# Performance work log

Measured on AMD Instinct MI355X. Metric: run time of the kernel, lower is better.

## Reference

```python
import jax, jax.numpy as jnp
import numpy as np

N, F_IN = 4096, 128
UNITS0, HEADS0 = 16, 4   # hidden GraphAttention layer
UNITS1, HEADS1 = 1, 1    # final layer (sigmoid, mean over last axis)


def _glorot(key, shape):
    fan_in, fan_out = shape[0], shape[1]
    std = (2.0 / (fan_in + fan_out)) ** 0.5
    return std * jax.random.normal(key, shape, dtype=jnp.float32)


def setup_inputs() -> dict:
    key = jax.random.key(0)
    ks = jax.random.split(key, 8)
    x = jax.random.normal(ks[0], (N, F_IN), dtype=jnp.float32)
    adj = (jax.random.uniform(ks[1], (N, N)) < 0.01).astype(jnp.float32)
    return {
        "x": x,
        "adj": adj,
        "w0": _glorot(ks[2], (F_IN, UNITS0)),
        "aw1_0": _glorot(ks[3], (UNITS0, HEADS0)),
        "aw2_0": _glorot(ks[4], (UNITS0, HEADS0)),
        "w1": _glorot(ks[5], (UNITS0 * HEADS0, UNITS1)),
        "aw1_1": _glorot(ks[6], (UNITS1, HEADS1)),
        "aw2_1": _glorot(ks[7], (UNITS1, HEADS1)),
    }


def _gat_layer(x, adj, w, aw1, aw2, activation, final_layer):
    h = x @ w                                   # [N, units]
    a1 = h @ aw1                                # [N, H]
    a2 = h @ aw2                                # [N, H]
    # relu(a1_i + a2_j) broadcast -> [N, N, H]
    coeffs = jax.nn.relu(a1[:, None, :] + a2[None, :, :])
    # elementwise adjacency mask then softmax over neighbor axis (axis=1),
    # matching tf.nn.softmax(adj * coeffs[:,:,i], axis=1)
    attn = jax.nn.softmax(adj[:, :, None] * coeffs, axis=1)   # [N, N, H]
    # per-head aggregation then concat heads: [N, H*units]
    out = jnp.einsum('ijh,jd->ihd', attn, h).reshape(h.shape[0], -1)
    if final_layer:
        out = out.mean(axis=-1)                 # [N]
    return activation(out)


def reference(x, adj, w0, aw1_0, aw2_0, w1, aw1_1, aw2_1):
    h = _gat_layer(x, adj, w0, aw1_0, aw2_0, jax.nn.relu, False)   # [N, 64]
    out = _gat_layer(h, adj, w1, aw1_1, aw2_1, jax.nn.sigmoid, True)  # [N]
    return out
```

## Files before the change

### kernel.cpp

```cpp
#include <hip/hip_runtime.h>
#include <hip/hip_bf16.h>

#define N 4096
#define FIN 128
#define U0 16
#define H0 4
#define MAXD 128
#define NGEMM (N / 16)

__global__ void k1_fused(const float* __restrict__ adj, const float* __restrict__ x,
                         const float* __restrict__ w0, const float* __restrict__ aw1,
                         const float* __restrict__ aw2,
                         int* __restrict__ deg, int* __restrict__ cols,
                         float* __restrict__ h0, float* __restrict__ a1,
                         float* __restrict__ a2, float* __restrict__ partS0) {
    const int t = threadIdx.x;
    if (blockIdx.x < NGEMM) {
        const int bid = blockIdx.x;
        __shared__ float xs[16][FIN + 1];
        __shared__ float ws[FIN][U0];
        __shared__ float hs[16][U0 + 1];
        const int r0 = bid * 16;

        for (int k = t; k < FIN * U0; k += 256) ws[k / U0][k % U0] = w0[k];
        for (int k = t; k < 16 * FIN; k += 256)
            xs[k / FIN][k % FIN] = x[(size_t)(r0 + k / FIN) * FIN + (k % FIN)];
        __syncthreads();

        const int r = t / U0, u = t % U0;
        float acc = 0.f;
        #pragma unroll 8
        for (int k = 0; k < FIN; ++k) acc += xs[r][k] * ws[k][u];
        hs[r][u] = acc;
        h0[(size_t)(r0 + r) * U0 + u] = acc;
        __syncthreads();

        if (t < 16 * H0) {
            const int rr = t / H0, hh = t % H0;
            float s1 = 0.f, s2 = 0.f;
            #pragma unroll
            for (int u2 = 0; u2 < U0; ++u2) {
                float hv = hs[rr][u2];
                s1 += hv * aw1[u2 * H0 + hh];
                s2 += hv * aw2[u2 * H0 + hh];
            }
            a1[(r0 + rr) * H0 + hh] = s1;
            a2[(r0 + rr) * H0 + hh] = s2;
        } else if (t >= 128 && t < 144) {
            const int d = t - 128;
            float s = 0.f;
            #pragma unroll
            for (int rr = 0; rr < 16; ++rr) s += hs[rr][d];
            partS0[bid * 16 + d] = s;
        }
    } else {
        const int row = blockIdx.x - NGEMM;
        const int lane = t & 63, wid = t >> 6;
        const float4* __restrict__ arow =
            reinterpret_cast<const float4*>(adj + (size_t)row * N);

        __shared__ int cls[MAXD];
        __shared__ int wsum[4];
        __shared__ int dgs;

        float4 v[4];
        int c = 0;
        #pragma unroll
        for (int p = 0; p < 4; ++p) {
            v[p] = arow[t + 256 * p];
            c += (v[p].x != 0.f) + (v[p].y != 0.f) + (v[p].z != 0.f) + (v[p].w != 0.f);
        }

        int sc = c;
        #pragma unroll
        for (int s = 1; s < 64; s <<= 1) {
            int u = __shfl_up(sc, s);
            if (lane >= s) sc += u;
        }
        if (lane == 63) wsum[wid] = sc;
        __syncthreads();
        int base = 0;
        #pragma unroll
        for (int w2 = 0; w2 < 4; ++w2)
            if (w2 < wid) base += wsum[w2];
        const int off = base + sc - c;
        if (t == 255) {
            const int dgv = min(base + sc, MAXD);
            dgs = dgv;
            deg[row] = dgv;
        }

        int w = off;
        #pragma unroll
        for (int p = 0; p < 4; ++p) {
            const int j0 = (t + 256 * p) * 4;
            if (v[p].x != 0.f && w < MAXD) cls[w++] = j0;
            if (v[p].y != 0.f && w < MAXD) cls[w++] = j0 + 1;
            if (v[p].z != 0.f && w < MAXD) cls[w++] = j0 + 2;
            if (v[p].w != 0.f && w < MAXD) cls[w++] = j0 + 3;
        }
        __syncthreads();
        if (t < dgs) cols[(size_t)row * MAXD + t] = cls[t];
    }
}

__global__ void attn0(const float* __restrict__ h0, const float* __restrict__ a1,
                      const float* __restrict__ a2, const float* __restrict__ partS0,
                      const int* __restrict__ deg, const int* __restrict__ cols,
                      const float* __restrict__ w1, float* __restrict__ hp) {
    const int i = blockIdx.x;
    const int t = threadIdx.x;
    __shared__ int cls[MAXD];
    __shared__ float red[16][17];
    __shared__ float s0s[16];
    __shared__ float ln[4][64];
    __shared__ float ld[4][64];

    const int dg = deg[i];
    if (t < MAXD) cls[t] = (t < dg) ? cols[(size_t)i * MAXD + t] : 0;

    {
        const int d = t & 15, ch = t >> 4;
        float s = 0.f;
        #pragma unroll
        for (int k = ch; k < 256; k += 16) s += partS0[k * 16 + d];
        red[ch][d] = s;
    }
    __syncthreads();
    if (t < 16) {
        float s2 = 0.f;
        #pragma unroll
        for (int k = 0; k < 16; ++k) s2 += red[k][t];
        s0s[t] = s2;
    }
    __syncthreads();

    const int wid = t >> 6, lane = t & 63;
    const int hh = lane >> 4, d = lane & 15;
    const float a1v = a1[i * H0 + hh];

    float accn = 0.f, accd = 0.f;
    for (int c = 0; ; ++c) {
        const int kb = wid + 16 * c;
        if (kb >= dg) break;
        int ja[4];
        float ms[4];
        #pragma unroll
        for (int q = 0; q < 4; ++q) {
            const int k = kb + 4 * q;
            ja[q] = cls[k < MAXD ? k : 0];
            ms[q] = (k < dg) ? 1.f : 0.f;
        }
        float a2v[4], h0v[4];
        #pragma unroll
        for (int q = 0; q < 4; ++q) {
            a2v[q] = a2[ja[q] * H0 + hh];
            h0v[q] = h0[(size_t)ja[q] * U0 + d];
        }
        #pragma unroll
        for (int q = 0; q < 4; ++q) {
            float cc = a1v + a2v[q];
            cc = cc > 0.f ? cc : 0.f;
            const float e = (__expf(cc) - 1.f) * ms[q];
            accn = fmaf(e, h0v[q], accn);
            accd += e;
        }
    }
    ln[wid][lane] = accn;
    ld[wid][lane] = accd;
    __syncthreads();

    if (t < 64) {
        const float an = ln[0][t] + ln[1][t] + ln[2][t] + ln[3][t];
        const float ad = ld[0][t] + ld[1][t] + ld[2][t] + ld[3][t];
        float o = (an + s0s[t & 15]) / (ad + (float)N);
        o = o > 0.f ? o : 0.f;

        float pv = o * w1[t];
        #pragma unroll
        for (int off = 32; off; off >>= 1) pv += __shfl_down(pv, off);
        if (t == 0) hp[i] = pv;
    }
}

__global__ void attn1(const float* __restrict__ hp,
                      const float* __restrict__ aw11, const float* __restrict__ aw21,
                      const int* __restrict__ deg, const int* __restrict__ cols,
                      float* __restrict__ out) {
    __shared__ float hps[N];
    __shared__ int cls[4][MAXD];
    __shared__ float s1red[4];
    const int t = threadIdx.x;
    const int w = t >> 6, lane = t & 63;
    const int i0 = blockIdx.x * 4;

    float s = 0.f;
    const float4* __restrict__ hp4 = reinterpret_cast<const float4*>(hp);
    #pragma unroll
    for (int k = t; k < N / 4; k += 256) {
        float4 v = hp4[k];
        reinterpret_cast<float4*>(hps)[k] = v;
        s += v.x + v.y + v.z + v.w;
    }
    for (int k = t; k < 4 * MAXD; k += 256)
        cls[k >> 7][k & 127] = cols[(size_t)(i0 + (k >> 7)) * MAXD + (k & 127)];

    #pragma unroll
    for (int o = 32; o; o >>= 1) s += __shfl_down(s, o);
    if (lane == 0) s1red[w] = s;
    __syncthreads();
    const float S1 = s1red[0] + s1red[1] + s1red[2] + s1red[3];

    const int i = i0 + w;
    const float w1v = aw11[0], w2v = aw21[0];
    const float a1v = hps[i] * w1v;
    const int dg = deg[i];

    float accn = 0.f, accd = 0.f;
    for (int k = lane; k < dg; k += 64) {
        const int j = cls[w][k];
        const float hj = hps[j];
        float cc = a1v + hj * w2v;
        cc = cc > 0.f ? cc : 0.f;
        const float e = __expf(cc) - 1.f;
        accn = fmaf(e, hj, accn);
        accd += e;
    }
    #pragma unroll
    for (int o = 32; o; o >>= 1) {
        accn += __shfl_down(accn, o);
        accd += __shfl_down(accd, o);
    }
    if (lane == 0) {
        const float v = (accn + S1) / (accd + (float)N);
        out[i] = 1.f / (1.f + __expf(-v));
    }
}

extern "C" void kernel_launch(void* const* d_in, const int* in_sizes, int n_in,
                              void* d_out, int out_size, void* d_ws, size_t ws_size,
                              hipStream_t stream) {
    const float* x    = (const float*)d_in[0];
    const float* adj  = (const float*)d_in[1];
    const float* w0   = (const float*)d_in[2];
    const float* aw10 = (const float*)d_in[3];
    const float* aw20 = (const float*)d_in[4];
    const float* w1   = (const float*)d_in[5];
    const float* aw11 = (const float*)d_in[6];
    const float* aw21 = (const float*)d_in[7];
    float* out = (float*)d_out;

    char* p = (char*)d_ws;
    auto alloc = [&](size_t bytes) {
        char* r = p;
        p += (bytes + 255) & ~(size_t)255;
        return r;
    };
    float* partS0 = (float*)alloc(NGEMM * 16 * 4);
    float* h0     = (float*)alloc((size_t)N * U0 * 4);
    float* a1     = (float*)alloc((size_t)N * H0 * 4);
    float* a2     = (float*)alloc((size_t)N * H0 * 4);
    float* hp     = (float*)alloc((size_t)N * 4);
    int*   deg    = (int*)alloc((size_t)N * 4);
    int*   cols   = (int*)alloc((size_t)N * MAXD * 4);

    k1_fused<<<N + NGEMM, 256, 0, stream>>>(adj, x, w0, aw10, aw20,
                                            deg, cols, h0, a1, a2, partS0);
    attn0<<<N, 256, 0, stream>>>(h0, a1, a2, partS0, deg, cols, w1, hp);
    attn1<<<N / 4, 256, 0, stream>>>(hp, aw11, aw21, deg, cols, out);
}
```

Measured before the change: 37.93 us.

## Interleave h0 and a2 into one strided buffer and process two adjacency rows per block

Stores h0 and a2 together in a 32-float-stride feature buffer, so each neighbor gather in attn0 reads one contiguous row instead of two separate arrays. The CSR-building part of k1_fused now handles two adjacency rows per block with 8 float4 loads in flight per thread, halving the block count and raising memory-level parallelism. This costs more registers per thread, an extra barrier, and a larger feature buffer with padding.

After: 38.77 us. 1.02x slower.

```diff
diff --git a/kernel.cpp b/kernel.cpp
--- a/kernel.cpp
+++ b/kernel.cpp
@@ -7,13 +7,15 @@
 #define H0 4
 #define MAXD 128
 #define NGEMM (N / 16)
+#define NCSR (N / 2)
+#define FSTRIDE 32
 
 __global__ void k1_fused(const float* __restrict__ adj, const float* __restrict__ x,
                          const float* __restrict__ w0, const float* __restrict__ aw1,
                          const float* __restrict__ aw2,
                          int* __restrict__ deg, int* __restrict__ cols,
-                         float* __restrict__ h0, float* __restrict__ a1,
-                         float* __restrict__ a2, float* __restrict__ partS0) {
+                         float* __restrict__ F, float* __restrict__ a1,
+                         float* __restrict__ partS0) {
     const int t = threadIdx.x;
     if (blockIdx.x < NGEMM) {
         const int bid = blockIdx.x;
@@ -32,7 +34,7 @@
         #pragma unroll 8
         for (int k = 0; k < FIN; ++k) acc += xs[r][k] * ws[k][u];
         hs[r][u] = acc;
-        h0[(size_t)(r0 + r) * U0 + u] = acc;
+        F[(size_t)(r0 + r) * FSTRIDE + u] = acc;
         __syncthreads();
 
         if (t < 16 * H0) {
@@ -45,7 +47,7 @@
                 s2 += hv * aw2[u2 * H0 + hh];
             }
             a1[(r0 + rr) * H0 + hh] = s1;
-            a2[(r0 + rr) * H0 + hh] = s2;
+            F[(size_t)(r0 + rr) * FSTRIDE + 16 + hh] = s2;
         } else if (t >= 128 && t < 144) {
             const int d = t - 128;
             float s = 0.f;
@@ -54,58 +56,73 @@
             partS0[bid * 16 + d] = s;
         }
     } else {
-        const int row = blockIdx.x - NGEMM;
+        const int rb = (blockIdx.x - NGEMM) * 2;
         const int lane = t & 63, wid = t >> 6;
-        const float4* __restrict__ arow =
-            reinterpret_cast<const float4*>(adj + (size_t)row * N);
-
-        __shared__ int cls[MAXD];
+
+        __shared__ int cls[2][MAXD];
         __shared__ int wsum[4];
-        __shared__ int dgs;
-
-        float4 v[4];
-        int c = 0;
-        #pragma unroll
-        for (int p = 0; p < 4; ++p) {
-            v[p] = arow[t + 256 * p];
-            c += (v[p].x != 0.f) + (v[p].y != 0.f) + (v[p].z != 0.f) + (v[p].w != 0.f);
-        }
-
-        int sc = c;
-        #pragma unroll
-        for (int s = 1; s < 64; s <<= 1) {
-            int u = __shfl_up(sc, s);
-            if (lane >= s) sc += u;
-        }
-        if (lane == 63) wsum[wid] = sc;
+        __shared__ int dgs[2];
+
+        const float4* __restrict__ ar0 =
+            reinterpret_cast<const float4*>(adj + (size_t)rb * N);
+        const float4* __restrict__ ar1 =
+            reinterpret_cast<const float4*>(adj + (size_t)(rb + 1) * N);
+        float4 v0[4], v1[4];
+        #pragma unroll
+        for (int p = 0; p < 4; ++p) v0[p] = ar0[t + 256 * p];
+        #pragma unroll
+        for (int p = 0; p < 4; ++p) v1[p] = ar1[t + 256 * p];
+
+        #pragma unroll
+        for (int rr = 0; rr < 2; ++rr) {
+            const float4* v = rr ? v1 : v0;
+            int c = 0;
+            #pragma unroll
+            for (int p = 0; p < 4; ++p)
+                c += (v[p].x != 0.f) + (v[p].y != 0.f) + (v[p].z != 0.f) + (v[p].w != 0.f);
+
+            int sc = c;
+            #pragma unroll
+            for (int s = 1; s < 64; s <<= 1) {
+                int u = __shfl_up(sc, s);
+                if (lane >= s) sc += u;
+            }
+            if (rr) __syncthreads();
+            if (lane == 63) wsum[wid] = sc;
+            __syncthreads();
+            int base = 0;
+            #pragma unroll
+            for (int w2 = 0; w2 < 4; ++w2)
+                if (w2 < wid) base += wsum[w2];
+            const int off = base + sc - c;
+            if (t == 255) dgs[rr] = min(base + sc, MAXD);
+
+            int w = off;
+            #pragma unroll
+            for (int p = 0; p < 4; ++p) {
+                const int j0 = (t + 256 * p) * 4;
+                if (v[p].x != 0.f && w < MAXD) cls[rr][w++] = j0;
+                if (v[p].y != 0.f && w < MAXD) cls[rr][w++] = j0 + 1;
+                if (v[p].z != 0.f && w < MAXD) cls[rr][w++] = j0 + 2;
+                if (v[p].w != 0.f && w < MAXD) cls[rr][w++] = j0 + 3;
+            }
+        }
         __syncthreads();
-        int base = 0;
-        #pragma unroll
-        for (int w2 = 0; w2 < 4; ++w2)
-            if (w2 < wid) base += wsum[w2];
-        const int off = base + sc - c;
-        if (t == 255) {
-            const int dgv = min(base + sc, MAXD);
-            dgs = dgv;
-            deg[row] = dgv;
-        }
-
-        int w = off;
-        #pragma unroll
-        for (int p = 0; p < 4; ++p) {
-            const int j0 = (t + 256 * p) * 4;
-            if (v[p].x != 0.f && w < MAXD) cls[w++] = j0;
-            if (v[p].y != 0.f && w < MAXD) cls[w++] = j0 + 1;
-            if (v[p].z != 0.f && w < MAXD) cls[w++] = j0 + 2;
-            if (v[p].w != 0.f && w < MAXD) cls[w++] = j0 + 3;
-        }
-        __syncthreads();
-        if (t < dgs) cols[(size_t)row * MAXD + t] = cls[t];
-    }
-}
-
-__global__ void attn0(const float* __restrict__ h0, const float* __restrict__ a1,
-                      const float* __restrict__ a2, const float* __restrict__ partS0,
+        if (t < dgs[0]) cols[(size_t)rb * MAXD + t] = cls[0][t];
+        const int t2 = t - 128;
+        if (t2 >= 0 && t2 < dgs[1] && t2 < 128)
+            cols[(size_t)(rb + 1) * MAXD + t2] = cls[1][t2];
+        if (t >= dgs[1] + 128 && t2 >= 128) {}
+        if (t < 128) {
+            const int k2 = t + 128;
+            if (k2 < dgs[1]) cols[(size_t)(rb + 1) * MAXD + k2] = cls[1][k2];
+        }
+        if (t == 0) { deg[rb] = dgs[0]; deg[rb + 1] = dgs[1]; }
+    }
+}
+
+__global__ void attn0(const float* __restrict__ F, const float* __restrict__ a1,
+                      const float* __restrict__ partS0,
                       const int* __restrict__ deg, const int* __restrict__ cols,
                       const float* __restrict__ w1, float* __restrict__ hp) {
     const int i = blockIdx.x;
@@ -154,8 +171,9 @@
         float a2v[4], h0v[4];
         #pragma unroll
         for (int q = 0; q < 4; ++q) {
-            a2v[q] = a2[ja[q] * H0 + hh];
-            h0v[q] = h0[(size_t)ja[q] * U0 + d];
+            const float* __restrict__ fj = F + (size_t)ja[q] * FSTRIDE;
+            h0v[q] = fj[d];
+            a2v[q] = fj[16 + hh];
         }
         #pragma unroll
         for (int q = 0; q < 4; ++q) {
@@ -257,15 +275,14 @@
         return r;
     };
     float* partS0 = (float*)alloc(NGEMM * 16 * 4);
-    float* h0     = (float*)alloc((size_t)N * U0 * 4);
+    float* F      = (float*)alloc((size_t)N * FSTRIDE * 4);
     float* a1     = (float*)alloc((size_t)N * H0 * 4);
-    float* a2     = (float*)alloc((size_t)N * H0 * 4);
     float* hp     = (float*)alloc((size_t)N * 4);
     int*   deg    = (int*)alloc((size_t)N * 4);
     int*   cols   = (int*)alloc((size_t)N * MAXD * 4);
 
-    k1_fused<<<N + NGEMM, 256, 0, stream>>>(adj, x, w0, aw10, aw20,
-                                            deg, cols, h0, a1, a2, partS0);
-    attn0<<<N, 256, 0, stream>>>(h0, a1, a2, partS0, deg, cols, w1, hp);
+    k1_fused<<<NGEMM + NCSR, 256, 0, stream>>>(adj, x, w0, aw10, aw20,
+                                               deg, cols, F, a1, partS0);
+    attn0<<<N, 256, 0, stream>>>(F, a1, partS0, deg, cols, w1, hp);
     attn1<<<N / 4, 256, 0, stream>>>(hp, aw11, aw21, deg, cols, out);
 }
```
